# Optimization experiments

Measured on AMD Instinct MI355X. Metric: run time of the kernel, lower is better.

## Reference

```python
import jax, jax.numpy as jnp
import numpy as np

B, T, C = 4, 2048, 1024
H = 16
D = C // H  # head_size = 64


def setup_inputs() -> dict:
    key = jax.random.key(0)
    ks = jax.random.split(key, 5)
    s = 0.02
    return {
        "x": jax.random.normal(ks[0], (B, T, C), dtype=jnp.float32),
        "Wq": jax.random.normal(ks[1], (C, C), dtype=jnp.float32) * s,
        "Wk": jax.random.normal(ks[2], (C, C), dtype=jnp.float32) * s,
        "Wv": jax.random.normal(ks[3], (C, C), dtype=jnp.float32) * s,
        "Wp": jax.random.normal(ks[4], (C, C), dtype=jnp.float32) * s,
        "bp": jnp.zeros((C,), dtype=jnp.float32),
    }


def reference(x, Wq, Wk, Wv, Wp, bp):
    Bq, Tq, Cq = x.shape
    # torch Linear: y = x @ W.T ; split into heads [B, H, T, D]
    def split(y):
        return y.reshape(Bq, Tq, H, D).transpose(0, 2, 1, 3)
    q = split(x @ Wq.T)
    k = split(x @ Wk.T)
    v = split(x @ Wv.T)
    # NOTE: original scales by C**-0.5 (full n_embed), not head_size**-0.5
    scale = Cq ** (-0.5)
    att = jnp.einsum('bhqd,bhkd->bhqk', q, k) * scale  # [B,H,T,T]
    causal = jnp.tril(jnp.ones((Tq, Tq), dtype=bool))
    att = jnp.where(causal[None, None, :, :], att, -jnp.inf)
    att = jax.nn.softmax(att, axis=-1)
    out = jnp.einsum('bhqk,bhkd->bhqd', att, v)  # [B,H,T,D]
    out = out.transpose(0, 2, 1, 3).reshape(Bq, Tq, Cq)
    return out @ Wp.T + bp
```

## Files before the change

### kernel.cpp

```cpp
#include <hip/hip_runtime.h>
#include <cstdint>
#include <cstddef>

typedef __attribute__((ext_vector_type(8))) __bf16 bf16x8;
typedef __attribute__((ext_vector_type(4))) __bf16 bf16x4;
typedef __attribute__((ext_vector_type(4))) float f32x4;
typedef __attribute__((ext_vector_type(16))) float f32x16;
typedef __attribute__((ext_vector_type(4))) unsigned uint4v;

#define B_ 4
#define T_ 2048
#define C_ 1024
#define H_ 16
#define D_ 64
#define NTILES_ (T_ / 32)
#define TILE_ELEMS_ 2048
#define BH_STRIDE_ ((size_t)NTILES_ * TILE_ELEMS_)

__device__ __forceinline__ float fexp2(float x) {
#if __has_builtin(__builtin_amdgcn_exp2f)
  return __builtin_amdgcn_exp2f(x);
#else
  return __expf(x * 0.69314718f);
#endif
}

__global__ __launch_bounds__(256) void castall(
    const float* __restrict__ x, const float* __restrict__ wq, const float* __restrict__ wk,
    const float* __restrict__ wv, const float* __restrict__ wp,
    __bf16* __restrict__ xb, __bf16* __restrict__ wqb, __bf16* __restrict__ wkb,
    __bf16* __restrict__ wvb, __bf16* __restrict__ wpb) {
  const int bid = blockIdx.x;
  const float* src;
  __bf16* dst;
  if (bid < 8192)       { src = x  + (size_t)bid * 1024;           dst = xb  + (size_t)bid * 1024; }
  else if (bid < 9216)  { src = wq + (size_t)(bid - 8192) * 1024;  dst = wqb + (size_t)(bid - 8192) * 1024; }
  else if (bid < 10240) { src = wk + (size_t)(bid - 9216) * 1024;  dst = wkb + (size_t)(bid - 9216) * 1024; }
  else if (bid < 11264) { src = wv + (size_t)(bid - 10240) * 1024; dst = wvb + (size_t)(bid - 10240) * 1024; }
  else                  { src = wp + (size_t)(bid - 11264) * 1024; dst = wpb + (size_t)(bid - 11264) * 1024; }
  const int i = threadIdx.x * 4;
  float4 f = *reinterpret_cast<const float4*>(src + i);
  bf16x4 o;
  o[0] = (__bf16)f.x; o[1] = (__bf16)f.y; o[2] = (__bf16)f.z; o[3] = (__bf16)f.w;
  *reinterpret_cast<bf16x4*>(dst + i) = o;
}

__device__ __forceinline__ void gload_lds16(const __bf16* g, __bf16* lds) {
  __builtin_amdgcn_global_load_lds(
      (const __attribute__((address_space(1))) void*)g,
      (__attribute__((address_space(3))) void*)lds, 16, 0, 0);
}

#define STAGE_A(BUFO, KT, HH)                                                         \
  do {                                                                                \
    const __bf16* s0_ = Agp + (size_t)(m0 + (HH) * 128 + srow) * 1024 + (KT) * 64 + sswz; \
    gload_lds16(s0_, LDSb + (BUFO) + (HH) * 8192 + w * 1024);                         \
    gload_lds16(s0_ + 8 * 1024, LDSb + (BUFO) + (HH) * 8192 + w * 1024 + 512);        \
  } while (0)
#define STAGE_B(BUFO, KT, HH)                                                         \
  do {                                                                                \
    const __bf16* s0_ = Bgp + (size_t)(n0 + (HH) * 128 + srow) * 1024 + (KT) * 64 + sswz; \
    gload_lds16(s0_, LDSb + 32768 + (BUFO) + (HH) * 8192 + w * 1024);                 \
    gload_lds16(s0_ + 8 * 1024, LDSb + 32768 + (BUFO) + (HH) * 8192 + w * 1024 + 512);\
  } while (0)
#define RD_A(M, KK) (*reinterpret_cast<const bf16x8*>(                                \
    LDSb + bufo + (wr * 128 + (M) * 16 + lr) * 64 + (((KK) * 32 + lg * 8) ^ ((lr & 7) * 8))))
#define RD_B(N, KK) (*reinterpret_cast<const bf16x8*>(                                \
    LDSb + 32768 + bufo + (wc * 64 + (N) * 16 + lr) * 64 + (((KK) * 32 + lg * 8) ^ ((lr & 7) * 8))))

#define GEMM8_KLOOP                                                                   \
  STAGE_A(0, 0, 0); STAGE_A(0, 0, 1);                                                 \
  STAGE_B(0, 0, 0); STAGE_B(0, 0, 1);                                                 \
  __builtin_amdgcn_sched_barrier(0);                                                  \
  asm volatile("s_waitcnt vmcnt(0)" ::: "memory");                                    \
  __builtin_amdgcn_s_barrier();                                                       \
  __builtin_amdgcn_sched_barrier(0);                                                  \
  for (int t = 0; t < 16; ++t) {                                                      \
    const int bufo = (t & 1) * 16384;                                                 \
    const int nbo = ((t + 1) & 1) * 16384;                                            \
    const bool st = t < 15;                                                           \
    _Pragma("unroll")                                                                 \
    for (int m = 0; m < 4; ++m) { afl[m][0] = RD_A(m, 0); afl[m][1] = RD_A(m, 1); }   \
    bfl[0][0] = RD_B(0, 0); bfl[0][1] = RD_B(0, 1);                                   \
    bfl[1][0] = RD_B(1, 0); bfl[1][1] = RD_B(1, 1);                                   \
    if (st) STAGE_A(nbo, t + 1, 0);                                                   \
    __builtin_amdgcn_s_setprio(1);                                                    \
    _Pragma("unroll")                                                                 \
    for (int kk = 0; kk < 2; ++kk)                                                    \
      _Pragma("unroll")                                                               \
      for (int m = 0; m < 4; ++m) {                                                   \
        acc[m][0] = __builtin_amdgcn_mfma_f32_16x16x32_bf16(afl[m][kk], bfl[0][kk], acc[m][0], 0, 0, 0); \
        acc[m][1] = __builtin_amdgcn_mfma_f32_16x16x32_bf16(afl[m][kk], bfl[1][kk], acc[m][1], 0, 0, 0); \
      }                                                                               \
    __builtin_amdgcn_s_setprio(0);                                                    \
    __builtin_amdgcn_s_barrier();                                                     \
    bfh[0][0] = RD_B(2, 0); bfh[0][1] = RD_B(2, 1);                                   \
    bfh[1][0] = RD_B(3, 0); bfh[1][1] = RD_B(3, 1);                                   \
    if (st) STAGE_A(nbo, t + 1, 1);                                                   \
    __builtin_amdgcn_s_setprio(1);                                                    \
    _Pragma("unroll")                                                                 \
    for (int kk = 0; kk < 2; ++kk)                                                    \
      _Pragma("unroll")                                                               \
      for (int m = 0; m < 4; ++m) {                                                   \
        acc[m][2] = __builtin_amdgcn_mfma_f32_16x16x32_bf16(afl[m][kk], bfh[0][kk], acc[m][2], 0, 0, 0); \
        acc[m][3] = __builtin_amdgcn_mfma_f32_16x16x32_bf16(afl[m][kk], bfh[1][kk], acc[m][3], 0, 0, 0); \
      }                                                                               \
    __builtin_amdgcn_s_setprio(0);                                                    \
    __builtin_amdgcn_s_barrier();                                                     \
    _Pragma("unroll")                                                                 \
    for (int m = 0; m < 4; ++m) { afl[m][0] = RD_A(m + 4, 0); afl[m][1] = RD_A(m + 4, 1); } \
    if (st) STAGE_B(nbo, t + 1, 0);                                                   \
    __builtin_amdgcn_s_setprio(1);                                                    \
    _Pragma("unroll")                                                                 \
    for (int kk = 0; kk < 2; ++kk)                                                    \
      _Pragma("unroll")                                                               \
      for (int m = 0; m < 4; ++m) {                                                   \
        acc[m + 4][0] = __builtin_amdgcn_mfma_f32_16x16x32_bf16(afl[m][kk], bfl[0][kk], acc[m + 4][0], 0, 0, 0); \
        acc[m + 4][1] = __builtin_amdgcn_mfma_f32_16x16x32_bf16(afl[m][kk], bfl[1][kk], acc[m + 4][1], 0, 0, 0); \
      }                                                                               \
    __builtin_amdgcn_s_setprio(0);                                                    \
    __builtin_amdgcn_s_barrier();                                                     \
    if (st) STAGE_B(nbo, t + 1, 1);                                                   \
    __builtin_amdgcn_s_setprio(1);                                                    \
    _Pragma("unroll")                                                                 \
    for (int kk = 0; kk < 2; ++kk)                                                    \
      _Pragma("unroll")                                                               \
      for (int m = 0; m < 4; ++m) {                                                   \
        acc[m + 4][2] = __builtin_amdgcn_mfma_f32_16x16x32_bf16(afl[m][kk], bfh[0][kk], acc[m + 4][2], 0, 0, 0); \
        acc[m + 4][3] = __builtin_amdgcn_mfma_f32_16x16x32_bf16(afl[m][kk], bfh[1][kk], acc[m + 4][3], 0, 0, 0); \
      }                                                                               \
    __builtin_amdgcn_s_setprio(0);                                                    \
    __builtin_amdgcn_sched_barrier(0);                                                \
    asm volatile("s_waitcnt vmcnt(0)" ::: "memory");                                  \
    __builtin_amdgcn_s_barrier();                                                     \
    __builtin_amdgcn_sched_barrier(0);                                                \
  }

__global__ __launch_bounds__(512, 2) void gemm_qkv8(
    const __bf16* __restrict__ Agp, const __bf16* __restrict__ Bgp,
    __bf16* __restrict__ qf, __bf16* __restrict__ kf, __bf16* __restrict__ vf) {
  __shared__ __bf16 LDSb[65536];
  const int tid = threadIdx.x;
  const int w = tid >> 6, l = tid & 63;
  const int wr = w >> 2, wc = w & 3;
  const int lr = l & 15, lg = l >> 4;
  int lin = blockIdx.y * 12 + blockIdx.x;
  lin = (lin & 7) * 48 + (lin >> 3);
  const int bx = lin % 12, by = lin / 12;
  const int m0 = by * 256, n0 = bx * 256;
  const int srow = w * 16 + (l >> 3);
  const int sswz = ((l & 7) ^ ((l >> 3) & 7)) * 8;

  f32x4 acc[8][4] = {};
  bf16x8 afl[4][2], bfl[2][2], bfh[2][2];

  GEMM8_KLOOP

  __bf16* wl = LDSb + w * 8192;
  const int colb = n0 + wc * 64;
  const int mat = colb >> 10;
  const int h = (colb >> 6) & 15;
  const int b = m0 >> 11;
  const float qsc = (mat == 0) ? 0.04508422f : 1.0f;
#pragma unroll
  for (int m = 0; m < 8; ++m) {
    const int rt = m >> 1;
#pragma unroll
    for (int n = 0; n < 4; ++n) {
      const int d = n * 16 + lr;
#pragma unroll
      for (int j = 0; j < 4; ++j) {
        const int rowloc = (m & 1) * 16 + lg * 4 + j;
        int off;
        if (mat < 2)
          off = ((d >> 4) & 3) * 512 + ((d >> 3) & 1) * 256 + rowloc * 8 + (d & 7);
        else
          off = (d >> 5) * 1024 + ((rowloc >> 4) & 1) * 512 + ((rowloc >> 3) & 1) * 256 +
                (d & 31) * 8 + (rowloc & 7);
        wl[rt * 2048 + off] = (__bf16)(acc[m][n][j] * qsc);
      }
    }
  }
  __bf16* dstbase = (mat == 0 ? qf : mat == 1 ? kf : vf) + (size_t)(b * 16 + h) * BH_STRIDE_;
  const int rt0 = ((m0 + wr * 128) >> 5) & 63;
#pragma unroll
  for (int rt = 0; rt < 4; ++rt)
#pragma unroll
    for (int c = 0; c < 4; ++c) {
      const bf16x8 vchunk = *reinterpret_cast<const bf16x8*>(wl + rt * 2048 + c * 512 + l * 8);
      *reinterpret_cast<bf16x8*>(dstbase + (size_t)(rt0 + rt) * TILE_ELEMS_ + c * 512 + l * 8) = vchunk;
    }
}

__global__ __launch_bounds__(512, 2) void gemm_proj8(
    const __bf16* __restrict__ Agp, const __bf16* __restrict__ Bgp,
    float* __restrict__ out, const float* __restrict__ bias) {
  __shared__ __bf16 LDSb[65536];
  const int tid = threadIdx.x;
  const int w = tid >> 6, l = tid & 63;
  const int wr = w >> 2, wc = w & 3;
  const int lr = l & 15, lg = l >> 4;
  int lin = blockIdx.y * 4 + blockIdx.x;
  lin = (lin & 7) * 16 + (lin >> 3);
  const int bx = lin & 3, by = lin >> 2;
  const int m0 = by * 256, n0 = bx * 256;
  const int srow = w * 16 + (l >> 3);
  const int sswz = ((l & 7) ^ ((l >> 3) & 7)) * 8;

  f32x4 acc[8][4] = {};
  bf16x8 afl[4][2], bfl[2][2], bfh[2][2];

  GEMM8_KLOOP

  const int colb = n0 + wc * 64;
#pragma unroll
  for (int m = 0; m < 8; ++m) {
    const int row = m0 + wr * 128 + (m >> 1) * 32 + (m & 1) * 16 + lg * 4;
#pragma unroll
    for (int n = 0; n < 4; ++n) {
      const int col = colb + n * 16 + lr;
      const float bv = bias[col];
#pragma unroll
      for (int j = 0; j < 4; ++j)
        out[(size_t)(row + j) * 1024 + col] = acc[m][n][j] + bv;
    }
  }
}

__device__ __forceinline__ unsigned pk2(float a, float b) {
  const unsigned short ua = __builtin_bit_cast(unsigned short, (__bf16)a);
  const unsigned short ub = __builtin_bit_cast(unsigned short, (__bf16)b);
  return (unsigned)ua | ((unsigned)ub << 16);
}

#define LOADKV(SFX, TT)                                                          \
  do {                                                                           \
    const __bf16* kp_ = kfb + (size_t)(TT) * TILE_ELEMS_ + lx8;                  \
    k##SFX##0 = *reinterpret_cast<const bf16x8*>(kp_);                           \
    k##SFX##1 = *reinterpret_cast<const bf16x8*>(kp_ + 512);                     \
    k##SFX##2 = *reinterpret_cast<const bf16x8*>(kp_ + 1024);                    \
    k##SFX##3 = *reinterpret_cast<const bf16x8*>(kp_ + 1536);                    \
    const __bf16* vp_ = vfb + (size_t)(TT) * TILE_ELEMS_ + lx8;                  \
    v##SFX##0 = *reinterpret_cast<const bf16x8*>(vp_);                           \
    v##SFX##1 = *reinterpret_cast<const bf16x8*>(vp_ + 512);                     \
    v##SFX##2 = *reinterpret_cast<const bf16x8*>(vp_ + 1024);                    \
    v##SFX##3 = *reinterpret_cast<const bf16x8*>(vp_ + 1536);                    \
  } while (0)

#define TILE(SFX, MASKED)                                                        \
  do {                                                                           \
    f32x16 s = {};                                                               \
    __builtin_amdgcn_s_setprio(1);                                               \
    s = __builtin_amdgcn_mfma_f32_32x32x16_bf16(k##SFX##0, qf[0], s, 0, 0, 0);   \
    s = __builtin_amdgcn_mfma_f32_32x32x16_bf16(k##SFX##1, qf[1], s, 0, 0, 0);   \
    s = __builtin_amdgcn_mfma_f32_32x32x16_bf16(k##SFX##2, qf[2], s, 0, 0, 0);   \
    s = __builtin_amdgcn_mfma_f32_32x32x16_bf16(k##SFX##3, qf[3], s, 0, 0, 0);   \
    __builtin_amdgcn_s_setprio(0);                                               \
    float sv[16];                                                                \
    _Pragma("unroll") for (int r = 0; r < 16; ++r) sv[r] = s[r];                 \
    if (MASKED) {                                                                \
      _Pragma("unroll") for (int r = 0; r < 16; ++r) {                           \
        const int kvloc = (r & 3) + 8 * (r >> 2) + 4 * hi;                       \
        sv[r] = (kvloc <= lane31) ? sv[r] : -1e30f;                              \
      }                                                                          \
    }                                                                            \
    _Pragma("unroll") for (int r = 0; r < 16; ++r) sv[r] = fexp2(sv[r]);         \
    unsigned pwv[8];                                                             \
    _Pragma("unroll") for (int ks = 0; ks < 2; ++ks) {                           \
      const unsigned X0 = pk2(sv[ks * 8 + 0], sv[ks * 8 + 1]);                   \
      const unsigned X1 = pk2(sv[ks * 8 + 2], sv[ks * 8 + 3]);                   \
      const unsigned Y0 = pk2(sv[ks * 8 + 4], sv[ks * 8 + 5]);                   \
      const unsigned Y1 = pk2(sv[ks * 8 + 6], sv[ks * 8 + 7]);                   \
      const unsigned sX0 = __shfl_xor(X0, 32);                                   \
      const unsigned sX1 = __shfl_xor(X1, 32);                                   \
      const unsigned sY0 = __shfl_xor(Y0, 32);                                   \
      const unsigned sY1 = __shfl_xor(Y1, 32);                                   \
      pwv[ks * 4 + 0] = hi ? sY0 : X0;                                           \
      pwv[ks * 4 + 1] = hi ? sY1 : X1;                                           \
      pwv[ks * 4 + 2] = hi ? Y0 : sX0;                                           \
      pwv[ks * 4 + 3] = hi ? Y1 : sX1;                                           \
    }                                                                            \
    const uint4v u0 = {pwv[0], pwv[1], pwv[2], pwv[3]};                          \
    const uint4v u1 = {pwv[4], pwv[5], pwv[6], pwv[7]};                          \
    const bf16x8 pf0 = __builtin_bit_cast(bf16x8, u0);                           \
    const bf16x8 pf1 = __builtin_bit_cast(bf16x8, u1);                           \
    __builtin_amdgcn_s_setprio(1);                                               \
    acc0 = __builtin_amdgcn_mfma_f32_32x32x16_bf16(v##SFX##0, pf0, acc0, 0, 0, 0); \
    acc0 = __builtin_amdgcn_mfma_f32_32x32x16_bf16(v##SFX##1, pf1, acc0, 0, 0, 0); \
    acc1 = __builtin_amdgcn_mfma_f32_32x32x16_bf16(v##SFX##2, pf0, acc1, 0, 0, 0); \
    acc1 = __builtin_amdgcn_mfma_f32_32x32x16_bf16(v##SFX##3, pf1, acc1, 0, 0, 0); \
    __builtin_amdgcn_s_setprio(0);                                               \
    float b8[8];                                                                 \
    _Pragma("unroll") for (int r = 0; r < 8; ++r) b8[r] = sv[2 * r] + sv[2 * r + 1]; \
    _Pragma("unroll") for (int r = 0; r < 4; ++r) b8[r] = b8[2 * r] + b8[2 * r + 1]; \
    l_run += (b8[0] + b8[1]) + (b8[2] + b8[3]);                                  \
  } while (0)

__global__ __launch_bounds__(512) void attn_fwd(const __bf16* __restrict__ qfr,
                                                const __bf16* __restrict__ kfr,
                                                const __bf16* __restrict__ vfr,
                                                __bf16* __restrict__ ao) {
  __shared__ float Pls[4 * 64 * 34];
  const int tid = threadIdx.x;
  const int w = tid >> 6, l = tid & 63;
  const int p = w >> 1, hf = w & 1;
  const int lane31 = l & 31, hi = l >> 5;
  const int bh = blockIdx.x & 63;
  const int qi = blockIdx.x >> 6;
  const int b = bh >> 4;
  const int qx = qi * 4 + p;
  const size_t rowbase = (size_t)b * T_;
  const int hoff = (bh & 15) * D_;
  const int lx8 = l * 8;
  const __bf16* qfb = qfr + (size_t)bh * BH_STRIDE_;
  const __bf16* kfb = kfr + (size_t)bh * BH_STRIDE_;
  const __bf16* vfb = vfr + (size_t)bh * BH_STRIDE_;
  float* pb = Pls + p * (64 * 34) + l * 34;

  for (int phase = 0; phase < 2; ++phase) {
    const int qg = (phase ? 63 - qx : qx) * 32;
    const int ntiles = (qg >> 5) + 1;
    const int nh = ntiles >> 1;
    const int tb = hf ? nh : 0;
    const int te = hf ? ntiles : nh;
    const int nt = te - tb;
    const bool dm = (hf == 1);

    bf16x8 qf[4];
    {
      const __bf16* qp = qfb + (size_t)(qg >> 5) * TILE_ELEMS_ + lx8;
#pragma unroll
      for (int t4 = 0; t4 < 4; ++t4) qf[t4] = *reinterpret_cast<const bf16x8*>(qp + t4 * 512);
    }

    f32x16 acc0 = {};
    f32x16 acc1 = {};
    float l_run = 0.f;

    bf16x8 kA0, kA1, kA2, kA3, vA0, vA1, vA2, vA3;
    bf16x8 kB0, kB1, kB2, kB3, vB0, vB1, vB2, vB3;

    if (nt > 0) {
      LOADKV(A, tb);
      int i = 0;
      for (; i + 1 < nt; ++i) {
        if ((i & 1) == 0) { LOADKV(B, tb + i + 1); TILE(A, false); }
        else              { LOADKV(A, tb + i + 1); TILE(B, false); }
      }
      if ((i & 1) == 0) TILE(A, dm);
      else              TILE(B, dm);
    }

    if (hf) {
#pragma unroll
      for (int r = 0; r < 16; ++r) { pb[r] = acc0[r]; pb[16 + r] = acc1[r]; }
      pb[32] = l_run;
    }
    __syncthreads();
    if (!hf) {
#pragma unroll
      for (int r = 0; r < 16; ++r) { acc0[r] += pb[r]; acc1[r] += pb[16 + r]; }
      l_run += pb[32];
      l_run += __shfl_xor(l_run, 32);
      const float rl = 1.0f / l_run;
      __bf16* op = ao + (rowbase + qg + lane31) * C_ + hoff + hi * 4;
#pragma unroll
      for (int dblk = 0; dblk < 2; ++dblk)
#pragma unroll
        for (int qd = 0; qd < 4; ++qd) {
          bf16x4 ov;
#pragma unroll
          for (int j = 0; j < 4; ++j) {
            const float av = (dblk == 0) ? acc0[qd * 4 + j] : acc1[qd * 4 + j];
            ov[j] = (__bf16)(av * rl);
          }
          *reinterpret_cast<bf16x4*>(op + dblk * 32 + qd * 8) = ov;
        }
    }
    __syncthreads();
  }
}

extern "C" void kernel_launch(void* const* d_in, const int* in_sizes, int n_in,
                              void* d_out, int out_size, void* d_ws, size_t ws_size,
                              hipStream_t stream) {
  const float* x  = (const float*)d_in[0];
  const float* Wq = (const float*)d_in[1];
  const float* Wk = (const float*)d_in[2];
  const float* Wv = (const float*)d_in[3];
  const float* Wp = (const float*)d_in[4];
  const float* bp = (const float*)d_in[5];
  float* out = (float*)d_out;

  const int NX = B_ * T_ * C_;
  const int NW = C_ * C_;

  __bf16* xb  = (__bf16*)d_ws;
  __bf16* wqb = xb + NX;
  __bf16* wkb = wqb + NW;
  __bf16* wvb = wkb + NW;
  __bf16* wpb = wvb + NW;
  __bf16* qf  = wpb + NW;
  __bf16* kf  = qf + NX;
  __bf16* vf  = kf + NX;
  __bf16* aob = xb;

  castall<<<12288, 256, 0, stream>>>(x, Wq, Wk, Wv, Wp, xb, wqb, wkb, wvb, wpb);

  gemm_qkv8<<<dim3(12, 32), 512, 0, stream>>>(xb, wqb, qf, kf, vf);
  attn_fwd<<<512, 512, 0, stream>>>(qf, kf, vf, aob);
  gemm_proj8<<<dim3(4, 32), 512, 0, stream>>>(aob, wpb, out, bp);
}
```

Baseline: 172.0 us.

## Halve GEMM N-tile to 128 and double grid for better CU utilization

Both the QKV and output-projection GEMMs now use 256x128 tiles with a 4x2 warp layout instead of 256x256 tiles with 2x4. The k-loop staging and fragment reads are reworked for the smaller B tile, LDS use drops, and the grids double. The goal is to fill all CUs, especially for the projection GEMM, which previously launched only 128 blocks. In exchange, A-tile reuse per block falls and global/L2 traffic rises.

```diff
diff --git a/kernel.cpp b/kernel.cpp
--- a/kernel.cpp
+++ b/kernel.cpp
@@ -51,83 +51,87 @@
       (__attribute__((address_space(3))) void*)lds, 16, 0, 0);
 }
 
-#define STAGE_A(BUFO, KT, HH)                                                         \
+#define ST_A41(BUFO, KT, HH)                                                          \
   do {                                                                                \
     const __bf16* s0_ = Agp + (size_t)(m0 + (HH) * 128 + srow) * 1024 + (KT) * 64 + sswz; \
     gload_lds16(s0_, LDSb + (BUFO) + (HH) * 8192 + w * 1024);                         \
     gload_lds16(s0_ + 8 * 1024, LDSb + (BUFO) + (HH) * 8192 + w * 1024 + 512);        \
   } while (0)
-#define STAGE_B(BUFO, KT, HH)                                                         \
+#define ST_B41(BUFO, KT)                                                              \
   do {                                                                                \
-    const __bf16* s0_ = Bgp + (size_t)(n0 + (HH) * 128 + srow) * 1024 + (KT) * 64 + sswz; \
-    gload_lds16(s0_, LDSb + 32768 + (BUFO) + (HH) * 8192 + w * 1024);                 \
-    gload_lds16(s0_ + 8 * 1024, LDSb + 32768 + (BUFO) + (HH) * 8192 + w * 1024 + 512);\
+    const __bf16* s0_ = Bgp + (size_t)(n0 + srow) * 1024 + (KT) * 64 + sswz;          \
+    gload_lds16(s0_, LDSb + 32768 + (BUFO) + w * 1024);                               \
+    gload_lds16(s0_ + 8 * 1024, LDSb + 32768 + (BUFO) + w * 1024 + 512);              \
   } while (0)
-#define RD_A(M, KK) (*reinterpret_cast<const bf16x8*>(                                \
-    LDSb + bufo + (wr * 128 + (M) * 16 + lr) * 64 + (((KK) * 32 + lg * 8) ^ ((lr & 7) * 8))))
-#define RD_B(N, KK) (*reinterpret_cast<const bf16x8*>(                                \
-    LDSb + 32768 + bufo + (wc * 64 + (N) * 16 + lr) * 64 + (((KK) * 32 + lg * 8) ^ ((lr & 7) * 8))))
-
-#define GEMM8_KLOOP                                                                   \
-  STAGE_A(0, 0, 0); STAGE_A(0, 0, 1);                                                 \
-  STAGE_B(0, 0, 0); STAGE_B(0, 0, 1);                                                 \
+#define RDA41(M, KK) (*reinterpret_cast<const bf16x8*>(                               \
+    LDSb + bufoA + (wr * 64 + (M) * 16 + lr) * 64 + (((KK) * 32 + lg * 8) ^ ((lr & 7) * 8))))
+#define RDB41(N, KK) (*reinterpret_cast<const bf16x8*>(                               \
+    LDSb + 32768 + bufoB + (wc * 64 + (N) * 16 + lr) * 64 + (((KK) * 32 + lg * 8) ^ ((lr & 7) * 8))))
+
+#define GEMM8_KLOOP_41                                                                \
+  ST_A41(0, 0, 0); ST_A41(0, 0, 1); ST_B41(0, 0);                                     \
   __builtin_amdgcn_sched_barrier(0);                                                  \
   asm volatile("s_waitcnt vmcnt(0)" ::: "memory");                                    \
   __builtin_amdgcn_s_barrier();                                                       \
   __builtin_amdgcn_sched_barrier(0);                                                  \
   for (int t = 0; t < 16; ++t) {                                                      \
-    const int bufo = (t & 1) * 16384;                                                 \
-    const int nbo = ((t + 1) & 1) * 16384;                                            \
+    const int bufoA = (t & 1) * 16384;                                                \
+    const int bufoB = (t & 1) * 8192;                                                 \
+    const int nboA = ((t + 1) & 1) * 16384;                                           \
+    const int nboB = ((t + 1) & 1) * 8192;                                            \
     const bool st = t < 15;                                                           \
-    _Pragma("unroll")                                                                 \
-    for (int m = 0; m < 4; ++m) { afl[m][0] = RD_A(m, 0); afl[m][1] = RD_A(m, 1); }   \
-    bfl[0][0] = RD_B(0, 0); bfl[0][1] = RD_B(0, 1);                                   \
-    bfl[1][0] = RD_B(1, 0); bfl[1][1] = RD_B(1, 1);                                   \
-    if (st) STAGE_A(nbo, t + 1, 0);                                                   \
+                       \
+    afA[0][0] = RDA41(0, 0); afA[0][1] = RDA41(0, 1);                                 \
+    afA[1][0] = RDA41(1, 0); afA[1][1] = RDA41(1, 1);                                 \
+    bfA[0][0] = RDB41(0, 0); bfA[0][1] = RDB41(0, 1);                                 \
+    bfA[1][0] = RDB41(1, 0); bfA[1][1] = RDB41(1, 1);                                 \
+    if (st) ST_A41(nboA, t + 1, 0);                                                   \
     __builtin_amdgcn_s_setprio(1);                                                    \
     _Pragma("unroll")                                                                 \
     for (int kk = 0; kk < 2; ++kk)                                                    \
       _Pragma("unroll")                                                               \
-      for (int m = 0; m < 4; ++m) {                                                   \
-        acc[m][0] = __builtin_amdgcn_mfma_f32_16x16x32_bf16(afl[m][kk], bfl[0][kk], acc[m][0], 0, 0, 0); \
-        acc[m][1] = __builtin_amdgcn_mfma_f32_16x16x32_bf16(afl[m][kk], bfl[1][kk], acc[m][1], 0, 0, 0); \
+      for (int m = 0; m < 2; ++m) {                                                   \
+        acc[m][0] = __builtin_amdgcn_mfma_f32_16x16x32_bf16(afA[m][kk], bfA[0][kk], acc[m][0], 0, 0, 0); \
+        acc[m][1] = __builtin_amdgcn_mfma_f32_16x16x32_bf16(afA[m][kk], bfA[1][kk], acc[m][1], 0, 0, 0); \
       }                                                                               \
     __builtin_amdgcn_s_setprio(0);                                                    \
     __builtin_amdgcn_s_barrier();                                                     \
-    bfh[0][0] = RD_B(2, 0); bfh[0][1] = RD_B(2, 1);                                   \
-    bfh[1][0] = RD_B(3, 0); bfh[1][1] = RD_B(3, 1);                                   \
-    if (st) STAGE_A(nbo, t + 1, 1);                                                   \
+                                \
+    bfB[0][0] = RDB41(2, 0); bfB[0][1] = RDB41(2, 1);                                 \
+    bfB[1][0] = RDB41(3, 0); bfB[1][1] = RDB41(3, 1);                                 \
+    if (st) ST_A41(nboA, t + 1, 1);                                                   \
     __builtin_amdgcn_s_setprio(1);                                                    \
     _Pragma("unroll")                                                                 \
     for (int kk = 0; kk < 2; ++kk)                                                    \
       _Pragma("unroll")                                                               \
-      for (int m = 0; m < 4; ++m) {                                                   \
-        acc[m][2] = __builtin_amdgcn_mfma_f32_16x16x32_bf16(afl[m][kk], bfh[0][kk], acc[m][2], 0, 0, 0); \
-        acc[m][3] = __builtin_amdgcn_mfma_f32_16x16x32_bf16(afl[m][kk], bfh[1][kk], acc[m][3], 0, 0, 0); \
+      for (int m = 0; m < 2; ++m) {                                                   \
+        acc[m][2] = __builtin_amdgcn_mfma_f32_16x16x32_bf16(afA[m][kk], bfB[0][kk], acc[m][2], 0, 0, 0); \
+        acc[m][3] = __builtin_amdgcn_mfma_f32_16x16x32_bf16(afA[m][kk], bfB[1][kk], acc[m][3], 0, 0, 0); \
       }                                                                               \
     __builtin_amdgcn_s_setprio(0);                                                    \
     __builtin_amdgcn_s_barrier();                                                     \
-    _Pragma("unroll")                                                                 \
-    for (int m = 0; m < 4; ++m) { afl[m][0] = RD_A(m + 4, 0); afl[m][1] = RD_A(m + 4, 1); } \
-    if (st) STAGE_B(nbo, t + 1, 0);                                                   \
+                                      \
+    afB[0][0] = RDA41(2, 0); afB[0][1] = RDA41(2, 1);                                 \
+    afB[1][0] = RDA41(3, 0); afB[1][1] = RDA41(3, 1);                                 \
+    if (st) ST_B41(nboB, t + 1);                                                      \
     __builtin_amdgcn_s_setprio(1);                                                    \
     _Pragma("unroll")                                                                 \
     for (int kk = 0; kk < 2; ++kk)                                                    \
       _Pragma("unroll")                                                               \
-      for (int m = 0; m < 4; ++m) {                                                   \
-        acc[m + 4][0] = __builtin_amdgcn_mfma_f32_16x16x32_bf16(afl[m][kk], bfl[0][kk], acc[m + 4][0], 0, 0, 0); \
-        acc[m + 4][1] = __builtin_amdgcn_mfma_f32_16x16x32_bf16(afl[m][kk], bfl[1][kk], acc[m + 4][1], 0, 0, 0); \
+      for (int m = 0; m < 2; ++m) {                                                   \
+        acc[m + 2][0] = __builtin_amdgcn_mfma_f32_16x16x32_bf16(afB[m][kk], bfA[0][kk], acc[m + 2][0], 0, 0, 0); \
+        acc[m + 2][1] = __builtin_amdgcn_mfma_f32_16x16x32_bf16(afB[m][kk], bfA[1][kk], acc[m + 2][1], 0, 0, 0); \
       }                                                                               \
     __builtin_amdgcn_s_setprio(0);                                                    \
     __builtin_amdgcn_s_barrier();                                                     \
-    if (st) STAGE_B(nbo, t + 1, 1);                                                   \
+                                      \
     __builtin_amdgcn_s_setprio(1);                                                    \
     _Pragma("unroll")                                                                 \
     for (int kk = 0; kk < 2; ++kk)                                                    \
       _Pragma("unroll")                                                               \
-      for (int m = 0; m < 4; ++m) {                                                   \
-        acc[m + 4][2] = __builtin_amdgcn_mfma_f32_16x16x32_bf16(afl[m][kk], bfh[0][kk], acc[m + 4][2], 0, 0, 0); \
-        acc[m + 4][3] = __builtin_amdgcn_mfma_f32_16x16x32_bf16(afl[m][kk], bfh[1][kk], acc[m + 4][3], 0, 0, 0); \
+      for (int m = 0; m < 2; ++m) {                                                   \
+        acc[m + 2][2] = __builtin_amdgcn_mfma_f32_16x16x32_bf16(afB[m][kk], bfB[0][kk], acc[m + 2][2], 0, 0, 0); \
+        acc[m + 2][3] = __builtin_amdgcn_mfma_f32_16x16x32_bf16(afB[m][kk], bfB[1][kk], acc[m + 2][3], 0, 0, 0); \
       }                                                                               \
     __builtin_amdgcn_s_setprio(0);                                                    \
     __builtin_amdgcn_sched_barrier(0);                                                \
@@ -139,52 +143,52 @@
 __global__ __launch_bounds__(512, 2) void gemm_qkv8(
     const __bf16* __restrict__ Agp, const __bf16* __restrict__ Bgp,
     __bf16* __restrict__ qf, __bf16* __restrict__ kf, __bf16* __restrict__ vf) {
-  __shared__ __bf16 LDSb[65536];
+  __shared__ __bf16 LDSb[49152];
   const int tid = threadIdx.x;
   const int w = tid >> 6, l = tid & 63;
-  const int wr = w >> 2, wc = w & 3;
+  const int wr = w >> 1, wc = w & 1;
   const int lr = l & 15, lg = l >> 4;
-  int lin = blockIdx.y * 12 + blockIdx.x;
-  lin = (lin & 7) * 48 + (lin >> 3);
-  const int bx = lin % 12, by = lin / 12;
-  const int m0 = by * 256, n0 = bx * 256;
+  int lin = blockIdx.y * 24 + blockIdx.x;
+  lin = (lin & 7) * 96 + (lin >> 3);
+  const int bx = lin % 24, by = lin / 24;
+  const int m0 = by * 256, n0 = bx * 128;
   const int srow = w * 16 + (l >> 3);
   const int sswz = ((l & 7) ^ ((l >> 3) & 7)) * 8;
 
-  f32x4 acc[8][4] = {};
-  bf16x8 afl[4][2], bfl[2][2], bfh[2][2];
-
-  GEMM8_KLOOP
-
-  __bf16* wl = LDSb + w * 8192;
+  f32x4 acc[4][4] = {};
+  bf16x8 afA[2][2], afB[2][2], bfA[2][2], bfB[2][2];
+
+  GEMM8_KLOOP_41
+
+  __bf16* wl = LDSb + w * 4096;
   const int colb = n0 + wc * 64;
   const int mat = colb >> 10;
   const int h = (colb >> 6) & 15;
   const int b = m0 >> 11;
   const float qsc = (mat == 0) ? 0.04508422f : 1.0f;
 #pragma unroll
-  for (int m = 0; m < 8; ++m) {
-    const int rt = m >> 1;
+  for (int mi = 0; mi < 4; ++mi) {
+    const int rt = mi >> 1;
 #pragma unroll
     for (int n = 0; n < 4; ++n) {
       const int d = n * 16 + lr;
 #pragma unroll
       for (int j = 0; j < 4; ++j) {
-        const int rowloc = (m & 1) * 16 + lg * 4 + j;
+        const int rowloc = (mi & 1) * 16 + lg * 4 + j;
         int off;
         if (mat < 2)
           off = ((d >> 4) & 3) * 512 + ((d >> 3) & 1) * 256 + rowloc * 8 + (d & 7);
         else
           off = (d >> 5) * 1024 + ((rowloc >> 4) & 1) * 512 + ((rowloc >> 3) & 1) * 256 +
                 (d & 31) * 8 + (rowloc & 7);
-        wl[rt * 2048 + off] = (__bf16)(acc[m][n][j] * qsc);
+        wl[rt * 2048 + off] = (__bf16)(acc[mi][n][j] * qsc);
       }
     }
   }
   __bf16* dstbase = (mat == 0 ? qf : mat == 1 ? kf : vf) + (size_t)(b * 16 + h) * BH_STRIDE_;
-  const int rt0 = ((m0 + wr * 128) >> 5) & 63;
-#pragma unroll
-  for (int rt = 0; rt < 4; ++rt)
+  const int rt0 = ((m0 + wr * 64) >> 5) & 63;
+#pragma unroll
+  for (int rt = 0; rt < 2; ++rt)
 #pragma unroll
     for (int c = 0; c < 4; ++c) {
       const bf16x8 vchunk = *reinterpret_cast<const bf16x8*>(wl + rt * 2048 + c * 512 + l * 8);
@@ -195,34 +199,34 @@
 __global__ __launch_bounds__(512, 2) void gemm_proj8(
     const __bf16* __restrict__ Agp, const __bf16* __restrict__ Bgp,
     float* __restrict__ out, const float* __restrict__ bias) {
-  __shared__ __bf16 LDSb[65536];
+  __shared__ __bf16 LDSb[49152];
   const int tid = threadIdx.x;
   const int w = tid >> 6, l = tid & 63;
-  const int wr = w >> 2, wc = w & 3;
+  const int wr = w >> 1, wc = w & 1;
   const int lr = l & 15, lg = l >> 4;
-  int lin = blockIdx.y * 4 + blockIdx.x;
-  lin = (lin & 7) * 16 + (lin >> 3);
-  const int bx = lin & 3, by = lin >> 2;
-  const int m0 = by * 256, n0 = bx * 256;
+  int lin = blockIdx.y * 8 + blockIdx.x;
+  lin = (lin & 7) * 32 + (lin >> 3);
+  const int bx = lin & 7, by = lin >> 3;
+  const int m0 = by * 256, n0 = bx * 128;
   const int srow = w * 16 + (l >> 3);
   const int sswz = ((l & 7) ^ ((l >> 3) & 7)) * 8;
 
-  f32x4 acc[8][4] = {};
-  bf16x8 afl[4][2], bfl[2][2], bfh[2][2];
-
-  GEMM8_KLOOP
+  f32x4 acc[4][4] = {};
+  bf16x8 afA[2][2], afB[2][2], bfA[2][2], bfB[2][2];
+
+  GEMM8_KLOOP_41
 
   const int colb = n0 + wc * 64;
 #pragma unroll
-  for (int m = 0; m < 8; ++m) {
-    const int row = m0 + wr * 128 + (m >> 1) * 32 + (m & 1) * 16 + lg * 4;
+  for (int mi = 0; mi < 4; ++mi) {
+    const int row = m0 + wr * 64 + mi * 16 + lg * 4;
 #pragma unroll
     for (int n = 0; n < 4; ++n) {
       const int col = colb + n * 16 + lr;
       const float bv = bias[col];
 #pragma unroll
       for (int j = 0; j < 4; ++j)
-        out[(size_t)(row + j) * 1024 + col] = acc[m][n][j] + bv;
+        out[(size_t)(row + j) * 1024 + col] = acc[mi][n][j] + bv;
     }
   }
 }
@@ -407,7 +411,7 @@
 
   castall<<<12288, 256, 0, stream>>>(x, Wq, Wk, Wv, Wp, xb, wqb, wkb, wvb, wpb);
 
-  gemm_qkv8<<<dim3(12, 32), 512, 0, stream>>>(xb, wqb, qf, kf, vf);
+  gemm_qkv8<<<dim3(24, 32), 512, 0, stream>>>(xb, wqb, qf, kf, vf);
   attn_fwd<<<512, 512, 0, stream>>>(qf, kf, vf, aob);
-  gemm_proj8<<<dim3(4, 32), 512, 0, stream>>>(aob, wpb, out, bp);
-}
+  gemm_proj8<<<dim3(8, 32), 512, 0, stream>>>(aob, wpb, out, bp);
+}
```

New measurement: 160.7 us. 6.6% less time.
